# Kernel tuning notes

Measured on AMD Instinct MI355X. Metric: run time of the kernel, lower is better.

The kernel has to match this reference:

```python
import jax, jax.numpy as jnp
import numpy as np

N_QUERIES = 33_554_432  # 32M query points (128 MB fp32)
N_KNOTS = 1024          # interpolation table size


def setup_inputs() -> dict:
    key = jax.random.key(0)
    k1, k2, k3 = jax.random.split(key, 3)
    # queries spread slightly beyond the knot range to exercise clamping branches
    x = jax.random.uniform(k1, (N_QUERIES,), dtype=jnp.float32, minval=-0.1, maxval=1.1)
    # unsorted knots (module sorts them in __init__; reference sorts too)
    x_points = jax.random.uniform(k2, (N_KNOTS,), dtype=jnp.float32)
    y_points = jax.random.normal(k3, (N_KNOTS,), dtype=jnp.float32)
    return {"x": x, "x_points": x_points, "y_points": y_points}


def reference(x, x_points, y_points):
    # __init__: sort knots by x, permute y accordingly
    order = jnp.argsort(x_points)
    xp = x_points[order]
    yp = y_points[order]
    n = xp.shape[0]
    # torch.searchsorted default (right=False) == side='left'
    idx = jnp.searchsorted(xp, x, side="left")  # [N], int
    # interior lerp uses (idx-1, idx); clip so gathers are in-range
    hi = jnp.clip(idx, 1, n - 1)
    lo = hi - 1
    x1, x2 = xp[lo], xp[hi]
    y1, y2 = yp[lo], yp[hi]
    interp = y1 + (x - x1) * (y2 - y1) / (x2 - x1)
    # boundary clamps: idx==0 -> y[0]; idx>=n -> y[-1]
    out = jnp.where(idx == 0, yp[0], jnp.where(idx >= n, yp[-1], interp))
    return out
```

## Files before the change

### kernel.cpp

```cpp
#include <hip/hip_runtime.h>
#include <math.h>

#define NK 1024
#define NB 4096

#define WS_QUAD_OFF 1028
#define WS_TAB_OFF  (1028 + 4096)

__device__ __forceinline__ int bucket_of(float x, float lo, float scale) {
    float t = __fmul_rn(__fsub_rn(x, lo), scale);
    int b = (int)t;
    b = b < 0 ? 0 : b;
    b = b > (NB - 1) ? (NB - 1) : b;
    return b;
}

__global__ __launch_bounds__(1024) void setup_kernel(
        const float* __restrict__ xp_in, const float* __restrict__ yp_in,
        float* __restrict__ wsf)
{
    __shared__ float2 kv[NK];
    __shared__ float2 kv2[NK];
    __shared__ int    hist[NB];
    __shared__ int    starts[NB];
    __shared__ int    iscan[NK];
    __shared__ float  red[NK];
    __shared__ int    flag;
    __shared__ float  s_lo, s_scale;

    const int t = threadIdx.x;
    float xv = xp_in[t];
    kv[t] = make_float2(xv, yp_in[t]);

    red[t] = xv; __syncthreads();
    for (int s = 512; s > 0; s >>= 1) {
        if (t < s) red[t] = fminf(red[t], red[t + s]);
        __syncthreads();
    }
    if (t == 0) s_lo = red[0];
    __syncthreads();
    red[t] = xv; __syncthreads();
    for (int s = 512; s > 0; s >>= 1) {
        if (t < s) red[t] = fmaxf(red[t], red[t + s]);
        __syncthreads();
    }
    if (t == 0) {
        float range = red[0] - s_lo;
        s_scale = (range > 0.0f) ? ((float)NB / range) : 0.0f;
    }
    __syncthreads();
    const float lo = s_lo, scale = s_scale;

    for (int i = t; i < NB; i += NK) hist[i] = 0;
    __syncthreads();
    const int bt = bucket_of(xv, lo, scale);
    atomicAdd(&hist[bt], 1);
    __syncthreads();

    int c0 = hist[4 * t], c1 = hist[4 * t + 1], c2 = hist[4 * t + 2], c3 = hist[4 * t + 3];
    int tot = c0 + c1 + c2 + c3;
    iscan[t] = tot; __syncthreads();
    for (int off = 1; off < NK; off <<= 1) {
        int v = (t >= off) ? iscan[t - off] : 0;
        __syncthreads();
        iscan[t] += v;
        __syncthreads();
    }
    int excl = iscan[t] - tot;
    starts[4 * t]     = excl;
    starts[4 * t + 1] = excl + c0;
    starts[4 * t + 2] = excl + c0 + c1;
    starts[4 * t + 3] = excl + c0 + c1 + c2;
    __syncthreads();

    for (int i = t; i < NB; i += NK) hist[i] = 0;
    __syncthreads();
    int pos = starts[bt] + atomicAdd(&hist[bt], 1);
    kv2[pos] = kv[t];
    __syncthreads();

    for (;;) {
        if (t == 0) flag = 0;
        __syncthreads();
        if (t < NK / 2) {
            int i0 = 2 * t;
            float2 a = kv2[i0], b = kv2[i0 + 1];
            if (a.x > b.x) { kv2[i0] = b; kv2[i0 + 1] = a; flag = 1; }
        }
        __syncthreads();
        if (t < NK / 2 - 1) {
            int i0 = 2 * t + 1;
            float2 a = kv2[i0], b = kv2[i0 + 1];
            if (a.x > b.x) { kv2[i0] = b; kv2[i0 + 1] = a; flag = 1; }
        }
        __syncthreads();
        if (!flag) break;
    }

    wsf[t] = kv2[t].x;
    if (t == 0) {
        wsf[NK]   = INFINITY;
        wsf[1025] = lo;
        wsf[1026] = scale;
    }
    float2 cur = kv2[t];
    float2 nxt = kv2[(t == NK - 1) ? (NK - 1) : (t + 1)];
    float4* qg = (float4*)(wsf + WS_QUAD_OFF);
    qg[t] = make_float4(cur.x, cur.y, nxt.x, nxt.y);
    unsigned short* tg = (unsigned short*)(wsf + WS_TAB_OFF);
    tg[4 * t]     = (unsigned short)starts[4 * t];
    tg[4 * t + 1] = (unsigned short)starts[4 * t + 1];
    tg[4 * t + 2] = (unsigned short)starts[4 * t + 2];
    tg[4 * t + 3] = (unsigned short)starts[4 * t + 3];
}

__device__ __forceinline__ float interp_one(
        float x, const float* __restrict__ sxp, const float4* __restrict__ quads,
        const unsigned short* __restrict__ table,
        float lo, float scale, float xp0, float xpN, float yp0, float ypN)
{
    int b = bucket_of(x, lo, scale);
    int j = table[b];
    while (sxp[j] < x) ++j;
    int hi = j < 1 ? 1 : (j > NK - 1 ? NK - 1 : j);
    float4 qd = quads[hi - 1];
    float r = __builtin_amdgcn_rcpf(qd.z - qd.x);
    float res = qd.y + (x - qd.x) * (qd.w - qd.y) * r;
    res = (x <= xp0) ? yp0 : res;
    res = (x >  xpN) ? ypN : res;
    return res;
}

__global__ __launch_bounds__(256, 4) void interp_kernel(
        const float4* __restrict__ xq, float4* __restrict__ out,
        const float* __restrict__ wsf, int n4)
{
    __shared__ float          sxp[NK + 1];
    __shared__ float4         quads[NK];
    __shared__ unsigned short table[NB];

    const int t = threadIdx.x;
    for (int i = t; i < NK + 1; i += 256) sxp[i] = wsf[i];
    const float lo = wsf[1025], scale = wsf[1026];
    const float4* qsrc = (const float4*)(wsf + WS_QUAD_OFF);
    for (int i = t; i < NK; i += 256) quads[i] = qsrc[i];
    const unsigned int* tsrc = (const unsigned int*)(wsf + WS_TAB_OFF);
    unsigned int* tdst = (unsigned int*)table;
    for (int i = t; i < NB / 2; i += 256) tdst[i] = tsrc[i];
    __syncthreads();

    const float xp0 = sxp[0], xpN = sxp[NK - 1];
    const float yp0 = quads[0].y, ypN = quads[NK - 1].y;

    int idx = blockIdx.x * 256 + t;
    const int stride = gridDim.x * 256;
    for (int q = idx; q < n4; q += stride) {
        float4 xv = xq[q];
        float4 r;
        r.x = interp_one(xv.x, sxp, quads, table, lo, scale, xp0, xpN, yp0, ypN);
        r.y = interp_one(xv.y, sxp, quads, table, lo, scale, xp0, xpN, yp0, ypN);
        r.z = interp_one(xv.z, sxp, quads, table, lo, scale, xp0, xpN, yp0, ypN);
        r.w = interp_one(xv.w, sxp, quads, table, lo, scale, xp0, xpN, yp0, ypN);
        out[q] = r;
    }
}

extern "C" void kernel_launch(void* const* d_in, const int* in_sizes, int n_in,
                              void* d_out, int out_size, void* d_ws, size_t ws_size,
                              hipStream_t stream)
{
    const float* x  = (const float*)d_in[0];
    const float* xp = (const float*)d_in[1];
    const float* yp = (const float*)d_in[2];
    float* out = (float*)d_out;
    float* wsf = (float*)d_ws;

    setup_kernel<<<1, 1024, 0, stream>>>(xp, yp, wsf);

    const int n4 = out_size / 4;
    interp_kernel<<<1280, 256, 0, stream>>>((const float4*)x, (float4*)out, wsf, n4);
}
```

Measured before the change: 237.1 us.

## Precompute per-bucket linear coefficients and bitonic-sort knots in setup

Setup now sorts the knots with a bitonic sort on packed keys, precomputes per-segment slopes, and builds a per-bucket table of linear coefficients. Buckets that hold no interior knot are marked as direct lerps, and NaN-marked buckets fall back to a global-memory linear scan. The interp kernel loads only this 32KB table into LDS, which cuts per-block LDS setup and the per-query search and divide. It also uses nontemporal vector loads and stores, a 2x unrolled grid-stride loop, and 512-thread blocks. Fallback queries read from global memory, and precomputed slope-times-offset can differ from the reference in the last bits.

Result: slower. 284.5 us (+20.0%).

```diff
diff --git a/kernel.cpp b/kernel.cpp
--- a/kernel.cpp
+++ b/kernel.cpp
@@ -4,8 +4,13 @@
 #define NK 1024
 #define NB 4096
 
-#define WS_QUAD_OFF 1028
-#define WS_TAB_OFF  (1028 + 4096)
+#define WS_SXP   0
+#define WS_META  1032
+#define WS_QUAD  1040
+#define WS_TAB   5136
+#define WS_FTAB  7184
+
+typedef float f4v __attribute__((ext_vector_type(4)));
 
 __device__ __forceinline__ int bucket_of(float x, float lo, float scale) {
     float t = __fmul_rn(__fsub_rn(x, lo), scale);
@@ -19,149 +24,172 @@
         const float* __restrict__ xp_in, const float* __restrict__ yp_in,
         float* __restrict__ wsf)
 {
-    __shared__ float2 kv[NK];
-    __shared__ float2 kv2[NK];
-    __shared__ int    hist[NB];
-    __shared__ int    starts[NB];
-    __shared__ int    iscan[NK];
-    __shared__ float  red[NK];
-    __shared__ int    flag;
-    __shared__ float  s_lo, s_scale;
+    __shared__ unsigned long long keys[NK];
+    __shared__ float sx[NK + 8];
+    __shared__ float sy[NK];
+    __shared__ float slp[NK];
+    __shared__ unsigned short tabs[NB];
 
     const int t = threadIdx.x;
+
     float xv = xp_in[t];
-    kv[t] = make_float2(xv, yp_in[t]);
-
-    red[t] = xv; __syncthreads();
-    for (int s = 512; s > 0; s >>= 1) {
-        if (t < s) red[t] = fminf(red[t], red[t + s]);
-        __syncthreads();
-    }
-    if (t == 0) s_lo = red[0];
-    __syncthreads();
-    red[t] = xv; __syncthreads();
-    for (int s = 512; s > 0; s >>= 1) {
-        if (t < s) red[t] = fmaxf(red[t], red[t + s]);
-        __syncthreads();
-    }
+    unsigned int fb  = __float_as_uint(xv);
+    unsigned int k32 = (fb & 0x80000000u) ? ~fb : (fb | 0x80000000u);
+    keys[t] = ((unsigned long long)k32 << 10) | (unsigned int)t;
+    __syncthreads();
+
+    for (int k = 2; k <= NK; k <<= 1) {
+        for (int j = k >> 1; j > 0; j >>= 1) {
+            int ixj = t ^ j;
+            if (ixj > t) {
+                unsigned long long a = keys[t], b = keys[ixj];
+                bool up = ((t & k) == 0);
+                if ((a > b) == up) { keys[t] = b; keys[ixj] = a; }
+            }
+            __syncthreads();
+        }
+    }
+
+    unsigned long long key = keys[t];
+    unsigned int s32 = (unsigned int)(key >> 10);
+    unsigned int xb  = (s32 & 0x80000000u) ? (s32 ^ 0x80000000u) : ~s32;
+    float xs = __uint_as_float(xb);
+    sx[t] = xs;
+    sy[t] = yp_in[(int)(key & (NK - 1))];
+    if (t < 8) sx[NK + t] = INFINITY;
+    __syncthreads();
+
+    const float lo  = sx[0];
+    const float xpN = sx[NK - 1];
+    float range = xpN - lo;
+    const float scale     = (range > 0.0f) ? ((float)NB / range) : 0.0f;
+    const float inv_scale = range * (1.0f / (float)NB);
+
+    slp[t] = (t < NK - 1) ? (sy[t + 1] - sy[t]) / (sx[t + 1] - sx[t]) : 0.0f;
+    __syncthreads();
+
+    for (int k = 0; k < 4; ++k) {
+        int b = 4 * t + k;
+        int loi = 0, hii = NK;
+        while (loi < hii) {
+            int mid = (loi + hii) >> 1;
+            if (bucket_of(sx[mid], lo, scale) < b) loi = mid + 1; else hii = mid;
+        }
+        tabs[b] = (unsigned short)loi;
+    }
+    __syncthreads();
+
+    float2*         ftabg = (float2*)(wsf + WS_FTAB);
+    unsigned short* tabg  = (unsigned short*)(wsf + WS_TAB);
+    for (int k = 0; k < 4; ++k) {
+        int b   = 4 * t + k;
+        int ib  = tabs[b];
+        int ib1 = (b == NB - 1) ? NK : tabs[b + 1];
+        int interior = ib1 - ib - (b == 0 ? 1 : 0) - (b == NB - 1 ? 1 : 0);
+        int hi = ib < 1 ? 1 : (ib > NK - 1 ? NK - 1 : ib);
+        float2 e;
+        if (interior > 0) {
+            e.x = __uint_as_float(0x7fc00000u);
+            e.y = 0.0f;
+        } else {
+            float a  = slp[hi - 1];
+            float bl = __fmaf_rn((float)b, inv_scale, lo);
+            e.x = a;
+            e.y = __fmaf_rn(bl - sx[hi - 1], a, sy[hi - 1]);
+        }
+        ftabg[b] = e;
+        tabg[b]  = (unsigned short)ib;
+    }
+
+    wsf[t] = sx[t];
+    if (t < 8) wsf[NK + t] = INFINITY;
+    float4* qg = (float4*)(wsf + WS_QUAD);
+    qg[t] = make_float4(sx[t], sy[t], slp[t], 0.0f);
     if (t == 0) {
-        float range = red[0] - s_lo;
-        s_scale = (range > 0.0f) ? ((float)NB / range) : 0.0f;
-    }
-    __syncthreads();
-    const float lo = s_lo, scale = s_scale;
-
-    for (int i = t; i < NB; i += NK) hist[i] = 0;
-    __syncthreads();
-    const int bt = bucket_of(xv, lo, scale);
-    atomicAdd(&hist[bt], 1);
-    __syncthreads();
-
-    int c0 = hist[4 * t], c1 = hist[4 * t + 1], c2 = hist[4 * t + 2], c3 = hist[4 * t + 3];
-    int tot = c0 + c1 + c2 + c3;
-    iscan[t] = tot; __syncthreads();
-    for (int off = 1; off < NK; off <<= 1) {
-        int v = (t >= off) ? iscan[t - off] : 0;
-        __syncthreads();
-        iscan[t] += v;
-        __syncthreads();
-    }
-    int excl = iscan[t] - tot;
-    starts[4 * t]     = excl;
-    starts[4 * t + 1] = excl + c0;
-    starts[4 * t + 2] = excl + c0 + c1;
-    starts[4 * t + 3] = excl + c0 + c1 + c2;
-    __syncthreads();
-
-    for (int i = t; i < NB; i += NK) hist[i] = 0;
-    __syncthreads();
-    int pos = starts[bt] + atomicAdd(&hist[bt], 1);
-    kv2[pos] = kv[t];
-    __syncthreads();
-
-    for (;;) {
-        if (t == 0) flag = 0;
-        __syncthreads();
-        if (t < NK / 2) {
-            int i0 = 2 * t;
-            float2 a = kv2[i0], b = kv2[i0 + 1];
-            if (a.x > b.x) { kv2[i0] = b; kv2[i0 + 1] = a; flag = 1; }
-        }
-        __syncthreads();
-        if (t < NK / 2 - 1) {
-            int i0 = 2 * t + 1;
-            float2 a = kv2[i0], b = kv2[i0 + 1];
-            if (a.x > b.x) { kv2[i0] = b; kv2[i0 + 1] = a; flag = 1; }
-        }
-        __syncthreads();
-        if (!flag) break;
-    }
-
-    wsf[t] = kv2[t].x;
-    if (t == 0) {
-        wsf[NK]   = INFINITY;
-        wsf[1025] = lo;
-        wsf[1026] = scale;
-    }
-    float2 cur = kv2[t];
-    float2 nxt = kv2[(t == NK - 1) ? (NK - 1) : (t + 1)];
-    float4* qg = (float4*)(wsf + WS_QUAD_OFF);
-    qg[t] = make_float4(cur.x, cur.y, nxt.x, nxt.y);
-    unsigned short* tg = (unsigned short*)(wsf + WS_TAB_OFF);
-    tg[4 * t]     = (unsigned short)starts[4 * t];
-    tg[4 * t + 1] = (unsigned short)starts[4 * t + 1];
-    tg[4 * t + 2] = (unsigned short)starts[4 * t + 2];
-    tg[4 * t + 3] = (unsigned short)starts[4 * t + 3];
+        wsf[WS_META + 0] = lo;
+        wsf[WS_META + 1] = inv_scale;
+        wsf[WS_META + 2] = scale;
+        wsf[WS_META + 3] = sy[0];
+        wsf[WS_META + 4] = sy[NK - 1];
+        wsf[WS_META + 5] = xpN;
+    }
 }
 
 __device__ __forceinline__ float interp_one(
-        float x, const float* __restrict__ sxp, const float4* __restrict__ quads,
-        const unsigned short* __restrict__ table,
-        float lo, float scale, float xp0, float xpN, float yp0, float ypN)
+        float x, const float2* __restrict__ ftab,
+        const float* __restrict__ gsxp, const float4* __restrict__ gquads,
+        const unsigned short* __restrict__ gtab,
+        float lo, float inv_scale, float scale, float xpN, float yp0, float ypN)
 {
     int b = bucket_of(x, lo, scale);
-    int j = table[b];
-    while (sxp[j] < x) ++j;
-    int hi = j < 1 ? 1 : (j > NK - 1 ? NK - 1 : j);
-    float4 qd = quads[hi - 1];
-    float r = __builtin_amdgcn_rcpf(qd.z - qd.x);
-    float res = qd.y + (x - qd.x) * (qd.w - qd.y) * r;
-    res = (x <= xp0) ? yp0 : res;
+    float2 e = ftab[b];
+    float bl  = __fmaf_rn((float)b, inv_scale, lo);
+    float res = __fmaf_rn(x - bl, e.x, e.y);
+    if (__builtin_isnan(e.x) && x > lo && x <= xpN) {
+        int j = gtab[b];
+        for (;;) {
+            float s0 = gsxp[j], s1 = gsxp[j + 1], s2 = gsxp[j + 2], s3 = gsxp[j + 3];
+            int c = (s0 < x) + (s1 < x) + (s2 < x) + (s3 < x);
+            j += c;
+            if (c < 4) break;
+        }
+        int hi = j < 1 ? 1 : (j > NK - 1 ? NK - 1 : j);
+        float4 qd = gquads[hi - 1];
+        res = __fmaf_rn(x - qd.x, qd.z, qd.y);
+    }
+    res = (x <= lo)  ? yp0 : res;
     res = (x >  xpN) ? ypN : res;
     return res;
 }
 
-__global__ __launch_bounds__(256, 4) void interp_kernel(
-        const float4* __restrict__ xq, float4* __restrict__ out,
+__global__ __launch_bounds__(512, 8) void interp_kernel(
+        const f4v* __restrict__ xq, f4v* __restrict__ out,
         const float* __restrict__ wsf, int n4)
 {
-    __shared__ float          sxp[NK + 1];
-    __shared__ float4         quads[NK];
-    __shared__ unsigned short table[NB];
-
+    __shared__ __align__(16) float2 ftab[NB];
     const int t = threadIdx.x;
-    for (int i = t; i < NK + 1; i += 256) sxp[i] = wsf[i];
-    const float lo = wsf[1025], scale = wsf[1026];
-    const float4* qsrc = (const float4*)(wsf + WS_QUAD_OFF);
-    for (int i = t; i < NK; i += 256) quads[i] = qsrc[i];
-    const unsigned int* tsrc = (const unsigned int*)(wsf + WS_TAB_OFF);
-    unsigned int* tdst = (unsigned int*)table;
-    for (int i = t; i < NB / 2; i += 256) tdst[i] = tsrc[i];
-    __syncthreads();
-
-    const float xp0 = sxp[0], xpN = sxp[NK - 1];
-    const float yp0 = quads[0].y, ypN = quads[NK - 1].y;
-
-    int idx = blockIdx.x * 256 + t;
-    const int stride = gridDim.x * 256;
-    for (int q = idx; q < n4; q += stride) {
-        float4 xv = xq[q];
-        float4 r;
-        r.x = interp_one(xv.x, sxp, quads, table, lo, scale, xp0, xpN, yp0, ypN);
-        r.y = interp_one(xv.y, sxp, quads, table, lo, scale, xp0, xpN, yp0, ypN);
-        r.z = interp_one(xv.z, sxp, quads, table, lo, scale, xp0, xpN, yp0, ypN);
-        r.w = interp_one(xv.w, sxp, quads, table, lo, scale, xp0, xpN, yp0, ypN);
-        out[q] = r;
+    {
+        const f4v* src = (const f4v*)(wsf + WS_FTAB);
+        f4v*       dst = (f4v*)ftab;
+        #pragma unroll
+        for (int i = 0; i < 4; ++i) dst[t + 512 * i] = src[t + 512 * i];
+    }
+    const float lo        = wsf[WS_META + 0];
+    const float inv_scale = wsf[WS_META + 1];
+    const float scale     = wsf[WS_META + 2];
+    const float yp0       = wsf[WS_META + 3];
+    const float ypN       = wsf[WS_META + 4];
+    const float xpN       = wsf[WS_META + 5];
+    const float*          gsxp   = wsf + WS_SXP;
+    const float4*         gquads = (const float4*)(wsf + WS_QUAD);
+    const unsigned short* gtab   = (const unsigned short*)(wsf + WS_TAB);
+    __syncthreads();
+
+    int q = blockIdx.x * 512 + t;
+    const int stride = gridDim.x * 512;
+    for (; q + stride < n4; q += 2 * stride) {
+        f4v xa = __builtin_nontemporal_load(&xq[q]);
+        f4v xb = __builtin_nontemporal_load(&xq[q + stride]);
+        f4v ra, rb;
+        ra.x = interp_one(xa.x, ftab, gsxp, gquads, gtab, lo, inv_scale, scale, xpN, yp0, ypN);
+        ra.y = interp_one(xa.y, ftab, gsxp, gquads, gtab, lo, inv_scale, scale, xpN, yp0, ypN);
+        ra.z = interp_one(xa.z, ftab, gsxp, gquads, gtab, lo, inv_scale, scale, xpN, yp0, ypN);
+        ra.w = interp_one(xa.w, ftab, gsxp, gquads, gtab, lo, inv_scale, scale, xpN, yp0, ypN);
+        __builtin_nontemporal_store(ra, &out[q]);
+        rb.x = interp_one(xb.x, ftab, gsxp, gquads, gtab, lo, inv_scale, scale, xpN, yp0, ypN);
+        rb.y = interp_one(xb.y, ftab, gsxp, gquads, gtab, lo, inv_scale, scale, xpN, yp0, ypN);
+        rb.z = interp_one(xb.z, ftab, gsxp, gquads, gtab, lo, inv_scale, scale, xpN, yp0, ypN);
+        rb.w = interp_one(xb.w, ftab, gsxp, gquads, gtab, lo, inv_scale, scale, xpN, yp0, ypN);
+        __builtin_nontemporal_store(rb, &out[q + stride]);
+    }
+    for (; q < n4; q += stride) {
+        f4v xa = __builtin_nontemporal_load(&xq[q]);
+        f4v ra;
+        ra.x = interp_one(xa.x, ftab, gsxp, gquads, gtab, lo, inv_scale, scale, xpN, yp0, ypN);
+        ra.y = interp_one(xa.y, ftab, gsxp, gquads, gtab, lo, inv_scale, scale, xpN, yp0, ypN);
+        ra.z = interp_one(xa.z, ftab, gsxp, gquads, gtab, lo, inv_scale, scale, xpN, yp0, ypN);
+        ra.w = interp_one(xa.w, ftab, gsxp, gquads, gtab, lo, inv_scale, scale, xpN, yp0, ypN);
+        __builtin_nontemporal_store(ra, &out[q]);
     }
 }
 
@@ -178,5 +206,5 @@
     setup_kernel<<<1, 1024, 0, stream>>>(xp, yp, wsf);
 
     const int n4 = out_size / 4;
-    interp_kernel<<<1280, 256, 0, stream>>>((const float4*)x, (float4*)out, wsf, n4);
-}
+    interp_kernel<<<1024, 512, 0, stream>>>((const f4v*)x, (f4v*)out, wsf, n4);
+}
```
